# Kernel tuning notes

Measured on AMD Instinct MI355X. Metric: run time of the kernel, lower is better.

Reference implementation:

```python
import jax, jax.numpy as jnp
import numpy as np

N, D_IN, D_OUT = 8192, 256, 64
NEG_INF = -9e15
LEAKY_SLOPE = 0.2  # tf.nn.leaky_relu default alpha


def setup_inputs() -> dict:
    key = jax.random.key(0)
    k1, k2, k3, k4 = jax.random.split(key, 4)
    x = jax.random.normal(k1, (N, D_IN), dtype=jnp.float32)
    adj = jax.random.randint(k2, (N, N), 0, 2, dtype=jnp.int32)
    W = jax.random.normal(k3, (D_IN, D_OUT), dtype=jnp.float32) * (1.0 / np.sqrt(D_IN))
    a = jax.random.normal(k4, (2 * D_OUT, 1), dtype=jnp.float32) * (1.0 / np.sqrt(2 * D_OUT))
    b = jnp.zeros((D_OUT,), dtype=jnp.float32)
    return {"x": x, "adj": adj, "W": W, "a": a, "b": b}


def reference(x, adj, W, a, b):
    # z: [N, D_OUT]
    z = x @ W
    # Additive GAT scores: e[i,j] = leaky_relu(a1.z_i + a2.z_j)
    # (equivalent to the tile/concat + matmul with a in the original,
    #  but avoids the [N*N, 2D] intermediate)
    a1 = a[:D_OUT, 0]   # [D_OUT]
    a2 = a[D_OUT:, 0]   # [D_OUT]
    si = z @ a1         # [N]
    sj = z @ a2         # [N]
    e = jax.nn.leaky_relu(si[:, None] + sj[None, :], negative_slope=LEAKY_SLOPE)
    masked = jnp.where(adj > 0, e, NEG_INF)
    alpha = jax.nn.softmax(masked, axis=1)  # row-wise over neighbors
    out = alpha @ z + b
    return jax.nn.relu(out)
```

## Files before the change

### kernel.cpp

```cpp
#include <hip/hip_runtime.h>
#include <hip/hip_bf16.h>

#define N 8192
#define DIN 256
#define DOUT 64
#define JSPLIT 16
#define JSPAN (N / JSPLIT)
#define NITILES (N / 64)
#define LEAKY 0.2f

typedef __attribute__((ext_vector_type(8))) short bf16x8;
typedef __attribute__((ext_vector_type(4))) float f32x4;

#define OFF_ZT   ((size_t)0)
#define OFF_SI   (OFF_ZT + (size_t)DOUT * N * 2)
#define OFF_SJ   (OFF_SI + (size_t)N * 4)
#define OFF_MAX  (OFF_SJ + (size_t)N * 4)
#define OFF_PDEN (OFF_MAX + 256)
#define OFF_PNUM (OFF_PDEN + (size_t)JSPLIT * N * 4)

static __device__ __forceinline__ short f2bf(float f) {
  union { __hip_bfloat16 h; short s; } u;
  u.h = __float2bfloat16(f);
  return u.s;
}

static __device__ __forceinline__ unsigned fkey(float f) {
  int b = __float_as_int(f);
  return (b < 0) ? ~(unsigned)b : ((unsigned)b | 0x80000000u);
}
static __device__ __forceinline__ float fdec(unsigned k) {
  int b = (k & 0x80000000u) ? (int)(k & 0x7fffffffu) : (int)~k;
  return __int_as_float(b);
}

__global__ __launch_bounds__(256) void gat_proj(
    const float* __restrict__ x, const float* __restrict__ W,
    const float* __restrict__ a, __hip_bfloat16* __restrict__ zT,
    float* __restrict__ si, float* __restrict__ sj,
    unsigned* __restrict__ mx) {
  __shared__ float wmx[4][2];
  const int lane = threadIdx.x & 63;
  const int wave = threadIdx.x >> 6;
  const int rowbase = blockIdx.x * 16 + wave * 4;
  float acc[4] = {0.f, 0.f, 0.f, 0.f};
  for (int k = 0; k < DIN; k += 4) {
    const float w0 = W[(k + 0) * DOUT + lane];
    const float w1 = W[(k + 1) * DOUT + lane];
    const float w2 = W[(k + 2) * DOUT + lane];
    const float w3 = W[(k + 3) * DOUT + lane];
#pragma unroll
    for (int r = 0; r < 4; ++r) {
      const float4 xv = *reinterpret_cast<const float4*>(&x[(size_t)(rowbase + r) * DIN + k]);
      acc[r] += xv.x * w0 + xv.y * w1 + xv.z * w2 + xv.w * w3;
    }
  }
  const float a1l = a[lane];
  const float a2l = a[DOUT + lane];
  float wm1 = -1e30f, wm2 = -1e30f;
#pragma unroll
  for (int r = 0; r < 4; ++r) {
    const int row = rowbase + r;
    zT[(size_t)lane * N + row] = __float2bfloat16(acc[r]);
    float v1 = acc[r] * a1l;
    float v2 = acc[r] * a2l;
#pragma unroll
    for (int m = 1; m < 64; m <<= 1) {
      v1 += __shfl_xor(v1, m);
      v2 += __shfl_xor(v2, m);
    }
    if (lane == 0) { si[row] = v1; sj[row] = v2; }
    wm1 = fmaxf(wm1, v1);
    wm2 = fmaxf(wm2, v2);
  }
  if (lane == 0) { wmx[wave][0] = wm1; wmx[wave][1] = wm2; }
  __syncthreads();
  if (threadIdx.x == 0) {
    float M1 = fmaxf(fmaxf(wmx[0][0], wmx[1][0]), fmaxf(wmx[2][0], wmx[3][0]));
    float M2 = fmaxf(fmaxf(wmx[0][1], wmx[1][1]), fmaxf(wmx[2][1], wmx[3][1]));
    atomicMax(mx + 0, fkey(M1));
    atomicMax(mx + 1, fkey(M2));
  }
}

__global__ __launch_bounds__(256, 6) void gat_main(
    const int* __restrict__ adj, const float* __restrict__ si,
    const float* __restrict__ sj, const __hip_bfloat16* __restrict__ zT,
    const unsigned* __restrict__ mx, float* __restrict__ pnum,
    float* __restrict__ pden) {
  const int lane = threadIdx.x & 63;
  const int wave = threadIdx.x >> 6;
  const int itile = blockIdx.x % NITILES;
  const int jchunk = blockIdx.x / NITILES;
  const int r16 = lane & 15;
  const int kgrp = lane >> 4;
  const int row = itile * 64 + wave * 16 + r16;

  const float tC = fdec(mx[0]) + fdec(mx[1]);
  const float C = tC > 0.f ? tC : LEAKY * tC;
  const float sir = si[row];

  const int jb0 = jchunk * JSPAN + kgrp * 8;
  const int* __restrict__ ap = adj + (size_t)row * N + jb0;
  const float* __restrict__ sp = sj + jb0;
  const __hip_bfloat16* __restrict__ zp = zT + (size_t)r16 * N + jb0;

  f32x4 acc0 = {0.f, 0.f, 0.f, 0.f};
  f32x4 acc1 = acc0, acc2 = acc0, acc3 = acc0;
  float dacc = 0.f;

  int4 a0 = *reinterpret_cast<const int4*>(ap);
  int4 a1 = *reinterpret_cast<const int4*>(ap + 4);

  const int NIT = JSPAN / 32;
#pragma unroll 1
  for (int it = 0; it < NIT; ++it) {
    const bf16x8 b0 = *reinterpret_cast<const bf16x8*>(zp);
    const bf16x8 b1 = *reinterpret_cast<const bf16x8*>(zp + 16 * N);
    const bf16x8 b2 = *reinterpret_cast<const bf16x8*>(zp + 32 * N);
    const bf16x8 b3 = *reinterpret_cast<const bf16x8*>(zp + 48 * N);
    const float4 s0 = *reinterpret_cast<const float4*>(sp);
    const float4 s1 = *reinterpret_cast<const float4*>(sp + 4);
    zp += 32;
    sp += 32;

    int4 na0 = a0, na1 = a1;
    if (it + 1 < NIT) {
      ap += 32;
      na0 = *reinterpret_cast<const int4*>(ap);
      na1 = *reinterpret_cast<const int4*>(ap + 4);
    }

    float p0, p1, p2, p3, p4, p5, p6, p7, t;
    t = sir + s0.x; t = fmaxf(t, LEAKY * t); p0 = (a0.x > 0) ? __expf(t - C) : 0.f;
    t = sir + s0.y; t = fmaxf(t, LEAKY * t); p1 = (a0.y > 0) ? __expf(t - C) : 0.f;
    t = sir + s0.z; t = fmaxf(t, LEAKY * t); p2 = (a0.z > 0) ? __expf(t - C) : 0.f;
    t = sir + s0.w; t = fmaxf(t, LEAKY * t); p3 = (a0.w > 0) ? __expf(t - C) : 0.f;
    t = sir + s1.x; t = fmaxf(t, LEAKY * t); p4 = (a1.x > 0) ? __expf(t - C) : 0.f;
    t = sir + s1.y; t = fmaxf(t, LEAKY * t); p5 = (a1.y > 0) ? __expf(t - C) : 0.f;
    t = sir + s1.z; t = fmaxf(t, LEAKY * t); p6 = (a1.z > 0) ? __expf(t - C) : 0.f;
    t = sir + s1.w; t = fmaxf(t, LEAKY * t); p7 = (a1.w > 0) ? __expf(t - C) : 0.f;

    dacc += ((p0 + p1) + (p2 + p3)) + ((p4 + p5) + (p6 + p7));

    bf16x8 afr;
    afr[0] = f2bf(p0); afr[1] = f2bf(p1); afr[2] = f2bf(p2); afr[3] = f2bf(p3);
    afr[4] = f2bf(p4); afr[5] = f2bf(p5); afr[6] = f2bf(p6); afr[7] = f2bf(p7);

    acc0 = __builtin_amdgcn_mfma_f32_16x16x32_bf16(afr, b0, acc0, 0, 0, 0);
    acc1 = __builtin_amdgcn_mfma_f32_16x16x32_bf16(afr, b1, acc1, 0, 0, 0);
    acc2 = __builtin_amdgcn_mfma_f32_16x16x32_bf16(afr, b2, acc2, 0, 0, 0);
    acc3 = __builtin_amdgcn_mfma_f32_16x16x32_bf16(afr, b3, acc3, 0, 0, 0);

    a0 = na0; a1 = na1;
  }

  dacc += __shfl_xor(dacc, 16);
  dacc += __shfl_xor(dacc, 32);
  if (lane < 16) pden[(size_t)jchunk * N + row] = dacc;

  float* np = pnum + ((size_t)jchunk * N + (size_t)itile * 64 + wave * 16) * DOUT;
  const f32x4 accs[4] = {acc0, acc1, acc2, acc3};
#pragma unroll
  for (int dt = 0; dt < 4; ++dt) {
#pragma unroll
    for (int r = 0; r < 4; ++r) {
      np[(kgrp * 4 + r) * DOUT + dt * 16 + r16] = accs[dt][r];
    }
  }
}

__global__ __launch_bounds__(256) void gat_combine(
    const float* __restrict__ pnum, const float* __restrict__ pden,
    const float* __restrict__ b, float* __restrict__ out) {
  const int idx = blockIdx.x * 256 + threadIdx.x;
  const int row = idx >> 6;
  const int d = idx & 63;
  float num = 0.f, den = 0.f;
#pragma unroll
  for (int s = 0; s < JSPLIT; ++s) num += pnum[(size_t)s * N * DOUT + idx];
#pragma unroll
  for (int s = 0; s < JSPLIT; ++s) den += pden[(size_t)s * N + row];
  const float o = num / den + b[d];
  out[idx] = o > 0.f ? o : 0.f;
}

extern "C" void kernel_launch(void* const* d_in, const int* in_sizes, int n_in,
                              void* d_out, int out_size, void* d_ws, size_t ws_size,
                              hipStream_t stream) {
  const float* x = (const float*)d_in[0];
  const int* adj = (const int*)d_in[1];
  const float* W = (const float*)d_in[2];
  const float* a = (const float*)d_in[3];
  const float* b = (const float*)d_in[4];
  float* out = (float*)d_out;
  char* ws = (char*)d_ws;

  __hip_bfloat16* zT = (__hip_bfloat16*)(ws + OFF_ZT);
  float* si = (float*)(ws + OFF_SI);
  float* sj = (float*)(ws + OFF_SJ);
  unsigned* mx = (unsigned*)(ws + OFF_MAX);
  float* pden = (float*)(ws + OFF_PDEN);
  float* pnum = (float*)(ws + OFF_PNUM);

  gat_proj<<<dim3(N / 16), dim3(256), 0, stream>>>(x, W, a, zT, si, sj, mx);
  gat_main<<<dim3(NITILES * JSPLIT), dim3(256), 0, stream>>>(adj, si, sj, zT, mx,
                                                             pnum, pden);
  gat_combine<<<dim3((N * DOUT) / 256), dim3(256), 0, stream>>>(pnum, pden, b, out);
}
```

Measured before the change: 461.3 us.

## Compress adjacency matrix to a bitmask before the attention pass

Adds a pre-pass kernel that reads the int32 adjacency matrix with fully coalesced loads and packs each group of 64 entries into one 64-bit word using wave ballots. The main attention kernel then reads one mask word per 64 columns instead of strided int4 loads of adjacency per lane, and drops its software prefetch. The full adjacency matrix is still read once per call, now by a separate launch, and the bitmask is written to and read back from workspace. The aim is to replace poorly coalesced adjacency reads inside the compute-heavy loop with a streaming pass.

After: 498.6 us. 1.08x slower.

```diff
diff --git a/kernel.cpp b/kernel.cpp
--- a/kernel.cpp
+++ b/kernel.cpp
@@ -7,6 +7,7 @@
 #define JSPLIT 16
 #define JSPAN (N / JSPLIT)
 #define NITILES (N / 64)
+#define NWORDS (N / 64)
 #define LEAKY 0.2f
 
 typedef __attribute__((ext_vector_type(8))) short bf16x8;
@@ -16,7 +17,8 @@
 #define OFF_SI   (OFF_ZT + (size_t)DOUT * N * 2)
 #define OFF_SJ   (OFF_SI + (size_t)N * 4)
 #define OFF_MAX  (OFF_SJ + (size_t)N * 4)
-#define OFF_PDEN (OFF_MAX + 256)
+#define OFF_MASK (OFF_MAX + 256)
+#define OFF_PDEN (OFF_MASK + (size_t)N * N / 8)
 #define OFF_PNUM (OFF_PDEN + (size_t)JSPLIT * N * 4)
 
 static __device__ __forceinline__ short f2bf(float f) {
@@ -83,8 +85,29 @@
   }
 }
 
+__global__ __launch_bounds__(256) void gat_compress(
+    const int* __restrict__ adj, unsigned long long* __restrict__ mask) {
+  const int lane = threadIdx.x & 63;
+  const size_t wid = (size_t)blockIdx.x * 4 + (threadIdx.x >> 6);
+  const size_t nw = (size_t)gridDim.x * 4;
+  const size_t total = (size_t)N * N / 64;
+  for (size_t w = wid * 4; w < total; w += nw * 4) {
+    const int v0 = adj[(w << 6) | lane];
+    const int v1 = adj[((w + 1) << 6) | lane];
+    const int v2 = adj[((w + 2) << 6) | lane];
+    const int v3 = adj[((w + 3) << 6) | lane];
+    const unsigned long long m0 = __ballot(v0 > 0);
+    const unsigned long long m1 = __ballot(v1 > 0);
+    const unsigned long long m2 = __ballot(v2 > 0);
+    const unsigned long long m3 = __ballot(v3 > 0);
+    if (lane == 0) {
+      mask[w] = m0; mask[w + 1] = m1; mask[w + 2] = m2; mask[w + 3] = m3;
+    }
+  }
+}
+
 __global__ __launch_bounds__(256, 6) void gat_main(
-    const int* __restrict__ adj, const float* __restrict__ si,
+    const unsigned long long* __restrict__ mask, const float* __restrict__ si,
     const float* __restrict__ sj, const __hip_bfloat16* __restrict__ zT,
     const unsigned* __restrict__ mx, float* __restrict__ pnum,
     float* __restrict__ pden) {
@@ -100,59 +123,53 @@
   const float C = tC > 0.f ? tC : LEAKY * tC;
   const float sir = si[row];
 
-  const int jb0 = jchunk * JSPAN + kgrp * 8;
-  const int* __restrict__ ap = adj + (size_t)row * N + jb0;
-  const float* __restrict__ sp = sj + jb0;
-  const __hip_bfloat16* __restrict__ zp = zT + (size_t)r16 * N + jb0;
+  const unsigned long long* __restrict__ mp =
+      mask + (size_t)row * NWORDS + (jchunk * JSPAN) / 64;
+  const float* __restrict__ sp = sj + jchunk * JSPAN + kgrp * 8;
+  const __hip_bfloat16* __restrict__ zp =
+      zT + (size_t)r16 * N + jchunk * JSPAN + kgrp * 8;
 
   f32x4 acc0 = {0.f, 0.f, 0.f, 0.f};
   f32x4 acc1 = acc0, acc2 = acc0, acc3 = acc0;
   float dacc = 0.f;
 
-  int4 a0 = *reinterpret_cast<const int4*>(ap);
-  int4 a1 = *reinterpret_cast<const int4*>(ap + 4);
-
-  const int NIT = JSPAN / 32;
 #pragma unroll 1
-  for (int it = 0; it < NIT; ++it) {
-    const bf16x8 b0 = *reinterpret_cast<const bf16x8*>(zp);
-    const bf16x8 b1 = *reinterpret_cast<const bf16x8*>(zp + 16 * N);
-    const bf16x8 b2 = *reinterpret_cast<const bf16x8*>(zp + 32 * N);
-    const bf16x8 b3 = *reinterpret_cast<const bf16x8*>(zp + 48 * N);
-    const float4 s0 = *reinterpret_cast<const float4*>(sp);
-    const float4 s1 = *reinterpret_cast<const float4*>(sp + 4);
-    zp += 32;
-    sp += 32;
-
-    int4 na0 = a0, na1 = a1;
-    if (it + 1 < NIT) {
-      ap += 32;
-      na0 = *reinterpret_cast<const int4*>(ap);
-      na1 = *reinterpret_cast<const int4*>(ap + 4);
-    }
-
-    float p0, p1, p2, p3, p4, p5, p6, p7, t;
-    t = sir + s0.x; t = fmaxf(t, LEAKY * t); p0 = (a0.x > 0) ? __expf(t - C) : 0.f;
-    t = sir + s0.y; t = fmaxf(t, LEAKY * t); p1 = (a0.y > 0) ? __expf(t - C) : 0.f;
-    t = sir + s0.z; t = fmaxf(t, LEAKY * t); p2 = (a0.z > 0) ? __expf(t - C) : 0.f;
-    t = sir + s0.w; t = fmaxf(t, LEAKY * t); p3 = (a0.w > 0) ? __expf(t - C) : 0.f;
-    t = sir + s1.x; t = fmaxf(t, LEAKY * t); p4 = (a1.x > 0) ? __expf(t - C) : 0.f;
-    t = sir + s1.y; t = fmaxf(t, LEAKY * t); p5 = (a1.y > 0) ? __expf(t - C) : 0.f;
-    t = sir + s1.z; t = fmaxf(t, LEAKY * t); p6 = (a1.z > 0) ? __expf(t - C) : 0.f;
-    t = sir + s1.w; t = fmaxf(t, LEAKY * t); p7 = (a1.w > 0) ? __expf(t - C) : 0.f;
-
-    dacc += ((p0 + p1) + (p2 + p3)) + ((p4 + p5) + (p6 + p7));
-
-    bf16x8 afr;
-    afr[0] = f2bf(p0); afr[1] = f2bf(p1); afr[2] = f2bf(p2); afr[3] = f2bf(p3);
-    afr[4] = f2bf(p4); afr[5] = f2bf(p5); afr[6] = f2bf(p6); afr[7] = f2bf(p7);
-
-    acc0 = __builtin_amdgcn_mfma_f32_16x16x32_bf16(afr, b0, acc0, 0, 0, 0);
-    acc1 = __builtin_amdgcn_mfma_f32_16x16x32_bf16(afr, b1, acc1, 0, 0, 0);
-    acc2 = __builtin_amdgcn_mfma_f32_16x16x32_bf16(afr, b2, acc2, 0, 0, 0);
-    acc3 = __builtin_amdgcn_mfma_f32_16x16x32_bf16(afr, b3, acc3, 0, 0, 0);
-
-    a0 = na0; a1 = na1;
+  for (int w = 0; w < JSPAN / 64; ++w) {
+    const unsigned long long mword = mp[w];
+#pragma unroll
+    for (int sub = 0; sub < 2; ++sub) {
+      const unsigned bits = (unsigned)(mword >> (sub * 32 + kgrp * 8)) & 0xffu;
+
+      const bf16x8 b0 = *reinterpret_cast<const bf16x8*>(zp);
+      const bf16x8 b1 = *reinterpret_cast<const bf16x8*>(zp + 16 * N);
+      const bf16x8 b2 = *reinterpret_cast<const bf16x8*>(zp + 32 * N);
+      const bf16x8 b3 = *reinterpret_cast<const bf16x8*>(zp + 48 * N);
+      const float4 s0 = *reinterpret_cast<const float4*>(sp);
+      const float4 s1 = *reinterpret_cast<const float4*>(sp + 4);
+      zp += 32;
+      sp += 32;
+
+      float p0, p1, p2, p3, p4, p5, p6, p7, t;
+      t = sir + s0.x; t = fmaxf(t, LEAKY * t); p0 = (bits & 1u)   ? __expf(t - C) : 0.f;
+      t = sir + s0.y; t = fmaxf(t, LEAKY * t); p1 = (bits & 2u)   ? __expf(t - C) : 0.f;
+      t = sir + s0.z; t = fmaxf(t, LEAKY * t); p2 = (bits & 4u)   ? __expf(t - C) : 0.f;
+      t = sir + s0.w; t = fmaxf(t, LEAKY * t); p3 = (bits & 8u)   ? __expf(t - C) : 0.f;
+      t = sir + s1.x; t = fmaxf(t, LEAKY * t); p4 = (bits & 16u)  ? __expf(t - C) : 0.f;
+      t = sir + s1.y; t = fmaxf(t, LEAKY * t); p5 = (bits & 32u)  ? __expf(t - C) : 0.f;
+      t = sir + s1.z; t = fmaxf(t, LEAKY * t); p6 = (bits & 64u)  ? __expf(t - C) : 0.f;
+      t = sir + s1.w; t = fmaxf(t, LEAKY * t); p7 = (bits & 128u) ? __expf(t - C) : 0.f;
+
+      dacc += ((p0 + p1) + (p2 + p3)) + ((p4 + p5) + (p6 + p7));
+
+      bf16x8 afr;
+      afr[0] = f2bf(p0); afr[1] = f2bf(p1); afr[2] = f2bf(p2); afr[3] = f2bf(p3);
+      afr[4] = f2bf(p4); afr[5] = f2bf(p5); afr[6] = f2bf(p6); afr[7] = f2bf(p7);
+
+      acc0 = __builtin_amdgcn_mfma_f32_16x16x32_bf16(afr, b0, acc0, 0, 0, 0);
+      acc1 = __builtin_amdgcn_mfma_f32_16x16x32_bf16(afr, b1, acc1, 0, 0, 0);
+      acc2 = __builtin_amdgcn_mfma_f32_16x16x32_bf16(afr, b2, acc2, 0, 0, 0);
+      acc3 = __builtin_amdgcn_mfma_f32_16x16x32_bf16(afr, b3, acc3, 0, 0, 0);
+    }
   }
 
   dacc += __shfl_xor(dacc, 16);
@@ -200,11 +217,13 @@
   float* si = (float*)(ws + OFF_SI);
   float* sj = (float*)(ws + OFF_SJ);
   unsigned* mx = (unsigned*)(ws + OFF_MAX);
+  unsigned long long* mask = (unsigned long long*)(ws + OFF_MASK);
   float* pden = (float*)(ws + OFF_PDEN);
   float* pnum = (float*)(ws + OFF_PNUM);
 
   gat_proj<<<dim3(N / 16), dim3(256), 0, stream>>>(x, W, a, zT, si, sj, mx);
-  gat_main<<<dim3(NITILES * JSPLIT), dim3(256), 0, stream>>>(adj, si, sj, zT, mx,
+  gat_compress<<<dim3(2048), dim3(256), 0, stream>>>(adj, mask);
+  gat_main<<<dim3(NITILES * JSPLIT), dim3(256), 0, stream>>>(mask, si, sj, zT, mx,
                                                              pnum, pden);
   gat_combine<<<dim3((N * DOUT) / 256), dim3(256), 0, stream>>>(pnum, pden, b, out);
 }
```

## Preload adjacency as coalesced ballot bitmasks before the MFMA loop

Applied to the files above, without the earlier changes.

Each wave now first reads its 16 rows of the adjacency chunk with fully coalesced 256-byte row loads and packs the mask bits with ballot into four 32-bit registers per lane. The main loop is then fully unrolled over 16 iterations and tests these bits instead of loading strided int4 pairs per row inside the loop. This targets the uncoalesced 32-byte-per-lane adjacency access pattern and the loop-carried prefetch. The cost is a serialized preload phase with no overlap against compute and higher register use from the full unroll.

New measurement: 480.9 us. 1.04x slower.

```diff
diff --git a/kernel.cpp b/kernel.cpp
--- a/kernel.cpp
+++ b/kernel.cpp
@@ -95,64 +95,82 @@
   const int r16 = lane & 15;
   const int kgrp = lane >> 4;
   const int row = itile * 64 + wave * 16 + r16;
+  const int jbase = jchunk * JSPAN;
+
+  unsigned bm0 = 0, bm1 = 0, bm2 = 0, bm3 = 0;
+  {
+    const int* __restrict__ abase =
+        adj + (size_t)(itile * 64 + wave * 16) * N + jbase;
+#pragma unroll 1
+    for (int rr = 0; rr < 16; ++rr) {
+      const int* __restrict__ ar = abase + (size_t)rr * N;
+#pragma unroll
+      for (int w = 0; w < 8; ++w) {
+        const int v = ar[w * 64 + lane];
+        const unsigned long long m = __ballot(v > 0);
+        const unsigned byte0 = (unsigned)(m >> (kgrp * 8)) & 0xffu;
+        const unsigned byte1 = (unsigned)(m >> (32 + kgrp * 8)) & 0xffu;
+        const unsigned contrib = (byte0 | (byte1 << 8)) << ((w & 1) * 16);
+        if (r16 == rr) {
+          if ((w >> 1) == 0) bm0 |= contrib;
+          else if ((w >> 1) == 1) bm1 |= contrib;
+          else if ((w >> 1) == 2) bm2 |= contrib;
+          else bm3 |= contrib;
+        }
+      }
+    }
+  }
 
   const float tC = fdec(mx[0]) + fdec(mx[1]);
   const float C = tC > 0.f ? tC : LEAKY * tC;
   const float sir = si[row];
 
-  const int jb0 = jchunk * JSPAN + kgrp * 8;
-  const int* __restrict__ ap = adj + (size_t)row * N + jb0;
-  const float* __restrict__ sp = sj + jb0;
-  const __hip_bfloat16* __restrict__ zp = zT + (size_t)r16 * N + jb0;
+  const float* __restrict__ sp = sj + jbase + kgrp * 8;
+  const __hip_bfloat16* __restrict__ zb0 = zT + (size_t)r16 * N + jbase + kgrp * 8;
+  const __hip_bfloat16* __restrict__ zb1 = zb0 + (size_t)16 * N;
+  const __hip_bfloat16* __restrict__ zb2 = zb0 + (size_t)32 * N;
+  const __hip_bfloat16* __restrict__ zb3 = zb0 + (size_t)48 * N;
 
   f32x4 acc0 = {0.f, 0.f, 0.f, 0.f};
   f32x4 acc1 = acc0, acc2 = acc0, acc3 = acc0;
   float dacc = 0.f;
 
-  int4 a0 = *reinterpret_cast<const int4*>(ap);
-  int4 a1 = *reinterpret_cast<const int4*>(ap + 4);
-
-  const int NIT = JSPAN / 32;
-#pragma unroll 1
-  for (int it = 0; it < NIT; ++it) {
-    const bf16x8 b0 = *reinterpret_cast<const bf16x8*>(zp);
-    const bf16x8 b1 = *reinterpret_cast<const bf16x8*>(zp + 16 * N);
-    const bf16x8 b2 = *reinterpret_cast<const bf16x8*>(zp + 32 * N);
-    const bf16x8 b3 = *reinterpret_cast<const bf16x8*>(zp + 48 * N);
-    const float4 s0 = *reinterpret_cast<const float4*>(sp);
-    const float4 s1 = *reinterpret_cast<const float4*>(sp + 4);
-    zp += 32;
-    sp += 32;
-
-    int4 na0 = a0, na1 = a1;
-    if (it + 1 < NIT) {
-      ap += 32;
-      na0 = *reinterpret_cast<const int4*>(ap);
-      na1 = *reinterpret_cast<const int4*>(ap + 4);
-    }
-
-    float p0, p1, p2, p3, p4, p5, p6, p7, t;
-    t = sir + s0.x; t = fmaxf(t, LEAKY * t); p0 = (a0.x > 0) ? __expf(t - C) : 0.f;
-    t = sir + s0.y; t = fmaxf(t, LEAKY * t); p1 = (a0.y > 0) ? __expf(t - C) : 0.f;
-    t = sir + s0.z; t = fmaxf(t, LEAKY * t); p2 = (a0.z > 0) ? __expf(t - C) : 0.f;
-    t = sir + s0.w; t = fmaxf(t, LEAKY * t); p3 = (a0.w > 0) ? __expf(t - C) : 0.f;
-    t = sir + s1.x; t = fmaxf(t, LEAKY * t); p4 = (a1.x > 0) ? __expf(t - C) : 0.f;
-    t = sir + s1.y; t = fmaxf(t, LEAKY * t); p5 = (a1.y > 0) ? __expf(t - C) : 0.f;
-    t = sir + s1.z; t = fmaxf(t, LEAKY * t); p6 = (a1.z > 0) ? __expf(t - C) : 0.f;
-    t = sir + s1.w; t = fmaxf(t, LEAKY * t); p7 = (a1.w > 0) ? __expf(t - C) : 0.f;
-
-    dacc += ((p0 + p1) + (p2 + p3)) + ((p4 + p5) + (p6 + p7));
-
-    bf16x8 afr;
-    afr[0] = f2bf(p0); afr[1] = f2bf(p1); afr[2] = f2bf(p2); afr[3] = f2bf(p3);
-    afr[4] = f2bf(p4); afr[5] = f2bf(p5); afr[6] = f2bf(p6); afr[7] = f2bf(p7);
-
-    acc0 = __builtin_amdgcn_mfma_f32_16x16x32_bf16(afr, b0, acc0, 0, 0, 0);
-    acc1 = __builtin_amdgcn_mfma_f32_16x16x32_bf16(afr, b1, acc1, 0, 0, 0);
-    acc2 = __builtin_amdgcn_mfma_f32_16x16x32_bf16(afr, b2, acc2, 0, 0, 0);
-    acc3 = __builtin_amdgcn_mfma_f32_16x16x32_bf16(afr, b3, acc3, 0, 0, 0);
-
-    a0 = na0; a1 = na1;
+#pragma unroll
+  for (int ph = 0; ph < 4; ++ph) {
+    const unsigned bmp = (ph == 0) ? bm0 : (ph == 1) ? bm1 : (ph == 2) ? bm2 : bm3;
+#pragma unroll
+    for (int sub = 0; sub < 4; ++sub) {
+      const int it = ph * 4 + sub;
+      const unsigned bits = (bmp >> (sub * 8)) & 0xffu;
+
+      const bf16x8 b0 = *reinterpret_cast<const bf16x8*>(zb0 + it * 32);
+      const bf16x8 b1 = *reinterpret_cast<const bf16x8*>(zb1 + it * 32);
+      const bf16x8 b2 = *reinterpret_cast<const bf16x8*>(zb2 + it * 32);
+      const bf16x8 b3 = *reinterpret_cast<const bf16x8*>(zb3 + it * 32);
+      const float4 s0 = *reinterpret_cast<const float4*>(sp + it * 32);
+      const float4 s1 = *reinterpret_cast<const float4*>(sp + it * 32 + 4);
+
+      float p0, p1, p2, p3, p4, p5, p6, p7, t;
+      t = sir + s0.x; t = fmaxf(t, LEAKY * t); p0 = (bits & 1u)   ? __expf(t - C) : 0.f;
+      t = sir + s0.y; t = fmaxf(t, LEAKY * t); p1 = (bits & 2u)   ? __expf(t - C) : 0.f;
+      t = sir + s0.z; t = fmaxf(t, LEAKY * t); p2 = (bits & 4u)   ? __expf(t - C) : 0.f;
+      t = sir + s0.w; t = fmaxf(t, LEAKY * t); p3 = (bits & 8u)   ? __expf(t - C) : 0.f;
+      t = sir + s1.x; t = fmaxf(t, LEAKY * t); p4 = (bits & 16u)  ? __expf(t - C) : 0.f;
+      t = sir + s1.y; t = fmaxf(t, LEAKY * t); p5 = (bits & 32u)  ? __expf(t - C) : 0.f;
+      t = sir + s1.z; t = fmaxf(t, LEAKY * t); p6 = (bits & 64u)  ? __expf(t - C) : 0.f;
+      t = sir + s1.w; t = fmaxf(t, LEAKY * t); p7 = (bits & 128u) ? __expf(t - C) : 0.f;
+
+      dacc += ((p0 + p1) + (p2 + p3)) + ((p4 + p5) + (p6 + p7));
+
+      bf16x8 afr;
+      afr[0] = f2bf(p0); afr[1] = f2bf(p1); afr[2] = f2bf(p2); afr[3] = f2bf(p3);
+      afr[4] = f2bf(p4); afr[5] = f2bf(p5); afr[6] = f2bf(p6); afr[7] = f2bf(p7);
+
+      acc0 = __builtin_amdgcn_mfma_f32_16x16x32_bf16(afr, b0, acc0, 0, 0, 0);
+      acc1 = __builtin_amdgcn_mfma_f32_16x16x32_bf16(afr, b1, acc1, 0, 0, 0);
+      acc2 = __builtin_amdgcn_mfma_f32_16x16x32_bf16(afr, b2, acc2, 0, 0, 0);
+      acc3 = __builtin_amdgcn_mfma_f32_16x16x32_bf16(afr, b3, acc3, 0, 0, 0);
+    }
   }
 
   dacc += __shfl_xor(dacc, 16);
```
